# Kernel optimization log

Hardware: AMD Instinct MI355X
Metric: run time of the kernel (lower is better)

Reference implementation:

```python
import jax, jax.numpy as jnp
import numpy as np

B, N, F, H, M = 128, 512, 63, 128, 2  # batch of trees, nodes/tree (post-order), feat dim, hidden, n modules
IN = F + 1            # features + treatment scalar
GATE_IN = IN + 2 * H  # cat(input, left_hidden, right_hidden)


def _build_tree(n, seed=0):
    """Random binary tree (forest) in post-order: children indices < parent index; -1 = absent."""
    rng = np.random.default_rng(seed)
    left = -np.ones(n, np.int32)
    right = -np.ones(n, np.int32)
    roots = []
    for t in range(n):
        r = rng.random()
        if len(roots) >= 2 and r < 0.6:
            right[t] = roots.pop()
            left[t] = roots.pop()
        elif len(roots) >= 1 and r < 0.85:
            left[t] = roots.pop()
        roots.append(t)
    return jnp.asarray(left), jnp.asarray(right)


def setup_inputs() -> dict:
    key = jax.random.key(0)
    k = jax.random.split(key, 8)
    left_child, right_child = _build_tree(N, seed=0)
    scale = 0.05
    return {
        "features": jax.random.normal(k[0], (B, N, F), jnp.float32),
        "treatment_id": jax.random.uniform(k[1], (B,), jnp.float32),
        "W_gate": jax.random.normal(k[2], (M, GATE_IN, 5 * H), jnp.float32) * scale,
        "b_gate": jax.random.normal(k[3], (M, 5 * H), jnp.float32) * scale,
        "W_out": jax.random.normal(k[4], (M, H, 1), jnp.float32) * scale,
        "b_out": jax.random.normal(k[5], (M, 1), jnp.float32) * scale,
        "module_idx": jax.random.randint(k[6], (B, N), 0, M, jnp.int32),
        "left_child": left_child,
        "right_child": right_child,
    }


def reference(features, treatment_id, W_gate, b_gate, W_out, b_out,
              module_idx, left_child, right_child):
    b_, n_, f_ = features.shape
    h = W_gate.shape[-1] // 5
    batch = jnp.arange(b_)
    # input tensor = cat(features, treatment) per node  -> [B, N, F+1]
    x = jnp.concatenate(
        [features, jnp.broadcast_to(treatment_id[:, None, None], (b_, n_, 1))], axis=-1)

    def fetch(buf, idx):
        # buf: [B, N, H]; idx: scalar child index (-1 -> zeros, matching torch zero init)
        v = buf[:, jnp.maximum(idx, 0)]
        return jnp.where(idx >= 0, v, jnp.zeros_like(v))

    def step(carry, xs):
        h_buf, c_buf = carry
        x_t, mod_t, lc, rc, t = xs  # x_t [B, IN], mod_t [B], lc/rc/t scalars
        lh, lcell = fetch(h_buf, lc), fetch(c_buf, lc)
        rh, rcell = fetch(h_buf, rc), fetch(c_buf, rc)
        combined = jnp.concatenate([x_t, lh, rh], axis=-1)  # [B, GATE_IN]
        # compute gates for all modules, select per-node module (per-operator fc_gate)
        gates = (jnp.einsum('bi,mio->bmo', combined, W_gate) + b_gate)[batch, mod_t]  # [B,5H]
        i_g, fl_g, fr_g, o_g, c_hat = jnp.split(gates, 5, axis=-1)
        cell = (jax.nn.sigmoid(i_g) * jnp.tanh(c_hat)
                + jax.nn.sigmoid(fl_g) * lcell
                + jax.nn.sigmoid(fr_g) * rcell)
        hidden = jax.nn.sigmoid(o_g) * jnp.tanh(cell)
        out = (jnp.einsum('bh,mh->bm', hidden, W_out[..., 0]) + b_out[:, 0][None])[batch, mod_t]
        h_buf = jax.lax.dynamic_update_slice(h_buf, hidden[:, None, :], (0, t, 0))
        c_buf = jax.lax.dynamic_update_slice(c_buf, cell[:, None, :], (0, t, 0))
        return (h_buf, c_buf), out

    xs = (jnp.swapaxes(x, 0, 1),          # [N, B, IN]
          jnp.swapaxes(module_idx, 0, 1),  # [N, B]
          left_child, right_child, jnp.arange(n_, dtype=jnp.int32))
    init = (jnp.zeros((b_, n_, h), features.dtype), jnp.zeros((b_, n_, h), features.dtype))
    _, outs = jax.lax.scan(step, init, xs)  # outs: [N, B]
    return outs.T  # [B, N] per-node scalar outputs in post-order
```

## Files before the change

kernel.cpp:

```cpp
#include <hip/hip_runtime.h>
#include <stdint.h>

#define BB 128
#define NN 512
#define FF 63
#define HH 128
#define C5H 640
#define MM 2
#define TPB 640
#define KK4 40
#define WP_DW_PER_M (KK4 * C5H * 4)
#define WP_DWORDS (MM * WP_DW_PER_M)
#define SCAP 32
#define NLDSG 6
#define NRREG 8
#define TT 16
#define GX_OFF ((size_t)4 << 20)
#define GX_BYTES ((size_t)BB * NN * C5H * 4)

__device__ __forceinline__ uint32_t f2bf_rne(float f) {
    uint32_t u = __float_as_uint(f);
    return (u + 0x7fffu + ((u >> 16) & 1u)) >> 16;
}
__device__ __forceinline__ float sigm_f(float x) { return 1.0f / (1.0f + __expf(-x)); }
__device__ __forceinline__ float tanh_f(float x) { return 1.0f - 2.0f / (__expf(2.0f * x) + 1.0f); }

__global__ void pack_w_kernel(const float* __restrict__ Wg, uint32_t* __restrict__ Wp) {
    int i = blockIdx.x * blockDim.x + threadIdx.x;
    if (i >= WP_DWORDS) return;
    int m   = i / WP_DW_PER_M;
    int d   = i % WP_DW_PER_M;
    int p   = d & 3;
    int col = (d >> 2) % C5H;
    int kk4 = d / (C5H * 4);
    int kk  = kk4 * 4 + p;
    float w0 = Wg[((size_t)m * 320 + 2 * kk    ) * C5H + col];
    float w1 = Wg[((size_t)m * 320 + 2 * kk + 1) * C5H + col];
    Wp[i] = f2bf_rne(w0) | (f2bf_rne(w1) << 16);
}

#define DOT2(acc, w, x) asm("v_dot2_f32_bf16 %0, %1, %2, %0" : "+v"(acc) : "v"(w), "v"(x))
#define DOT4G(acc, wq, xp) do { uint4 _x = *(const uint4*)(xp); \
    DOT2(acc, (wq).x, _x.x); DOT2(acc, (wq).y, _x.y); \
    DOT2(acc, (wq).z, _x.z); DOT2(acc, (wq).w, _x.w); } while (0)

#define BAR_L()  do { asm volatile("s_waitcnt lgkmcnt(0)" ::: "memory"); \
                      __builtin_amdgcn_s_barrier(); \
                      asm volatile("" ::: "memory"); } while (0)

__device__ __forceinline__ float seg_dot(float acc, const uint4* __restrict__ w4,
                                         int g0, int ng, const uint32_t* __restrict__ cf) {
#pragma unroll 4
    for (int g = 0; g < ng; ++g) {
        uint4 w = w4[(size_t)(g0 + g) * C5H];
        uint4 x = *(const uint4*)(cf + 4 * g);
        DOT2(acc, w.x, x.x);
        DOT2(acc, w.y, x.y);
        DOT2(acc, w.z, x.z);
        DOT2(acc, w.w, x.w);
    }
    return acc;
}

__global__ __launch_bounds__(TPB, 1) void gx_kernel(
    const float* __restrict__ feat, const float* __restrict__ treat,
    const float* __restrict__ bgate, const int* __restrict__ modidx,
    const uint32_t* __restrict__ Wp, float* __restrict__ gx)
{
    __shared__ __align__(16) uint32_t comb16[TT][32];
    __shared__ int mod16[TT];
    const int tid = threadIdx.x;
    const int b   = blockIdx.x;
    const int t0  = blockIdx.y * TT;
    const float trt = treat[b];

    uint4 wx0[8], wx1[8];
    {
        const uint4* w40 = (const uint4*)Wp + tid;
        const uint4* w41 = (const uint4*)Wp + (size_t)KK4 * C5H + tid;
#pragma unroll
        for (int g = 0; g < 8; ++g) wx0[g] = w40[(size_t)g * C5H];
#pragma unroll
        for (int g = 0; g < 8; ++g) wx1[g] = w41[(size_t)g * C5H];
    }
    if (tid < TT * 32) {
        int tt = tid >> 5, l = tid & 31;
        const float* fr = feat + ((size_t)b * NN + t0 + tt) * FF;
        float a = fr[2 * l];
        float c = (l == 31) ? trt : fr[2 * l + 1];
        comb16[tt][l] = f2bf_rne(a) | (f2bf_rne(c) << 16);
    }
    if (tid < TT) mod16[tid] = modidx[b * NN + t0 + tid];
    __syncthreads();

    const float bg0 = bgate[tid], bg1 = bgate[C5H + tid];
    for (int tt = 0; tt < TT; ++tt) {
        const int m = mod16[tt];
        float acc;
        if (m == 0) {
            acc = bg0;
#pragma unroll
            for (int g = 0; g < 8; ++g) DOT4G(acc, wx0[g], &comb16[tt][4 * g]);
        } else {
            acc = bg1;
#pragma unroll
            for (int g = 0; g < 8; ++g) DOT4G(acc, wx1[g], &comb16[tt][4 * g]);
        }
        gx[((size_t)b * NN + t0 + tt) * C5H + tid] = acc;
    }
}

template<int USEGX>
__global__ __launch_bounds__(TPB, 1) void tree_lstm_kernel(
    const float* __restrict__ feat, const float* __restrict__ treat,
    const float* __restrict__ bgate, const float* __restrict__ wout,
    const float* __restrict__ bout, const int* __restrict__ modidx,
    const int* __restrict__ lchild, const int* __restrict__ rchild,
    const uint32_t* __restrict__ Wp, const float* __restrict__ gx,
    float* __restrict__ out)
{
    __shared__ __align__(16) ushort h_live[SCAP * HH];
    __shared__ float               c_live[SCAP * HH];
    __shared__ uint32_t wlds[MM][NLDSG][4][C5H];
    __shared__ float gatesf[C5H];
    __shared__ float partial[HH];
    __shared__ float wo_l[MM * HH];
    __shared__ float bo_l[MM];
    __shared__ unsigned char code_l[NN];
    __shared__ __align__(16) uint32_t comb_x[USEGX ? 4 : 32];
    __shared__ float bg_l[USEGX ? 1 : MM * C5H];

    const int tid = threadIdx.x;
    const int b   = blockIdx.x;
    const float trt = treat[b];

    for (int i = tid; i < MM * HH; i += TPB) wo_l[i] = wout[i];
    if (tid < MM) bo_l[tid] = bout[tid];
    if (!USEGX) { for (int i = tid; i < MM * C5H; i += TPB) bg_l[i] = bgate[i]; }
    for (int i = tid; i < NN; i += TPB) {
        int lc = lchild[i], rc = rchild[i];
        code_l[i] = (unsigned char)((modidx[b * NN + i] & 1) |
                                    ((lc >= 0) ? 2 : 0) | ((rc >= 0) ? 4 : 0));
    }
    for (int i = tid; i < MM * NLDSG * 4 * C5H; i += TPB) {
        int m  = i / (NLDSG * 4 * C5H);
        int r  = i % (NLDSG * 4 * C5H);
        int j  = r / (4 * C5H);
        int p  = (r / C5H) & 3;
        int c  = r % C5H;
        wlds[m][j][p][c] =
            Wp[(size_t)m * WP_DW_PER_M + (size_t)(8 + j) * 2560 + c * 4 + p];
    }

    uint4 wr0[NRREG], wr1[NRREG];
    {
        const uint4* w40 = (const uint4*)Wp + tid;
        const uint4* w41 = (const uint4*)Wp + (size_t)KK4 * C5H + tid;
#pragma unroll
        for (int j = 0; j < NRREG; ++j) wr0[j] = w40[(size_t)(24 + j) * C5H];
#pragma unroll
        for (int j = 0; j < NRREG; ++j) wr1[j] = w41[(size_t)(24 + j) * C5H];
    }

    float fx0 = 0.f, fx1 = 0.f;
    if (!USEGX && tid < 32) {
        fx0 = feat[(size_t)b * NN * FF + 2 * tid];
        if (tid < 31) fx1 = feat[(size_t)b * NN * FF + 2 * tid + 1];
    }
    const float* gxp = gx + (size_t)b * NN * C5H + tid;
    float gx_next = USEGX ? gxp[0] : 0.f;
    __syncthreads();

    int sp = 0;
    for (int t = 0; t < NN; ++t) {
        const int code = code_l[t];
        const int m = code & 1;
        const bool hasL = (code & 2) != 0, hasR = (code & 4) != 0;
        const int rh_slot = sp - 1;
        const int lh_slot = hasR ? sp - 2 : sp - 1;
        const int new_slot = hasL ? lh_slot : sp;

        if (!USEGX) {
            if (tid < 32) {
                comb_x[tid] = f2bf_rne(fx0) | (f2bf_rne((tid == 31) ? trt : fx1) << 16);
                if (t + 1 < NN) {
                    fx0 = feat[((size_t)b * NN + t + 1) * FF + 2 * tid];
                    if (tid < 31) fx1 = feat[((size_t)b * NN + t + 1) * FF + 2 * tid + 1];
                }
            }
            BAR_L();
        }

        {
            const uint4* w4 = (const uint4*)Wp + (size_t)m * (KK4 * C5H) + tid;
            float acc;
            if (USEGX) {
                acc = gx_next;
                if (t + 1 < NN) gx_next = gxp[(size_t)(t + 1) * C5H];
            } else {
                acc = bg_l[m * C5H + tid];
                acc = seg_dot(acc, w4, 0, 8, comb_x);
            }
            if (hasL) {
                const uint32_t* hl = (const uint32_t*)&h_live[lh_slot * HH];
                const uint32_t* wt = &wlds[m][0][0][0] + tid;
#pragma unroll
                for (int j = 0; j < NLDSG; ++j) {
                    uint4 w;
                    w.x = wt[(size_t)(4 * j    ) * C5H];
                    w.y = wt[(size_t)(4 * j + 1) * C5H];
                    w.z = wt[(size_t)(4 * j + 2) * C5H];
                    w.w = wt[(size_t)(4 * j + 3) * C5H];
                    DOT4G(acc, w, hl + 4 * j);
                }
                acc = seg_dot(acc, w4, 8 + NLDSG, 16 - NLDSG, hl + 4 * NLDSG);
            }
            if (hasR) {
                const uint32_t* hr = (const uint32_t*)&h_live[rh_slot * HH];
                if (m == 0) {
#pragma unroll
                    for (int j = 0; j < NRREG; ++j) DOT4G(acc, wr0[j], hr + 4 * j);
                } else {
#pragma unroll
                    for (int j = 0; j < NRREG; ++j) DOT4G(acc, wr1[j], hr + 4 * j);
                }
                acc = seg_dot(acc, w4, 24 + NRREG, 16 - NRREG, hr + 4 * NRREG);
            }
            gatesf[tid] = (tid < 4 * HH) ? sigm_f(acc) : tanh_f(acc);
        }
        BAR_L();

        if (tid < HH) {
            float s_i  = gatesf[tid];
            float s_fl = gatesf[HH + tid];
            float s_fr = gatesf[2 * HH + tid];
            float s_o  = gatesf[3 * HH + tid];
            float th   = gatesf[4 * HH + tid];
            float pcl = hasL ? c_live[lh_slot * HH + tid] : 0.0f;
            float pcr = hasR ? c_live[rh_slot * HH + tid] : 0.0f;
            float cell = s_i * th + s_fl * pcl + s_fr * pcr;
            float hid  = s_o * tanh_f(cell);
            c_live[new_slot * HH + tid] = cell;
            h_live[new_slot * HH + tid] = (ushort)f2bf_rne(hid);
            partial[tid] = hid * wo_l[m * HH + tid];
        }
        BAR_L();

        if (tid < 64) {
            float s = partial[tid] + partial[tid + 64];
#pragma unroll
            for (int off = 32; off; off >>= 1) s += __shfl_down(s, off, 64);
            if (tid == 0) out[(size_t)b * NN + t] = s + bo_l[m];
        }

        sp = hasR ? sp - 1 : (hasL ? sp : sp + 1);
    }
}

extern "C" void kernel_launch(void* const* d_in, const int* in_sizes, int n_in,
                              void* d_out, int out_size, void* d_ws, size_t ws_size,
                              hipStream_t stream) {
    const float* feat   = (const float*)d_in[0];
    const float* treat  = (const float*)d_in[1];
    const float* Wg     = (const float*)d_in[2];
    const float* bgate  = (const float*)d_in[3];
    const float* wout   = (const float*)d_in[4];
    const float* bout   = (const float*)d_in[5];
    const int*   modidx = (const int*)d_in[6];
    const int*   lchild = (const int*)d_in[7];
    const int*   rchild = (const int*)d_in[8];

    uint32_t* Wp = (uint32_t*)d_ws;
    float* gxbuf = (float*)((char*)d_ws + GX_OFF);
    float* out = (float*)d_out;
    const bool use_gx = ws_size >= GX_OFF + GX_BYTES;

    pack_w_kernel<<<(WP_DWORDS + 255) / 256, 256, 0, stream>>>(Wg, Wp);
    if (use_gx) {
        gx_kernel<<<dim3(BB, NN / TT), TPB, 0, stream>>>(feat, treat, bgate, modidx, Wp, gxbuf);
        tree_lstm_kernel<1><<<BB, TPB, 0, stream>>>(feat, treat, bgate, wout, bout,
                                                    modidx, lchild, rchild, Wp, gxbuf, out);
    } else {
        tree_lstm_kernel<0><<<BB, TPB, 0, stream>>>(feat, treat, bgate, wout, bout,
                                                    modidx, lchild, rchild, Wp, gxbuf, out);
    }
}
```

Before: 863.1 us.

## Defer output projection out of recurrent loop, store hidden to gx scratch

In the precomputed-gx path, each step now writes its hidden vector into the gx row it has already consumed, and the per-node output dot product runs in a parallel pass after the loop. This takes the reduction and its shuffle work off the serial critical path. The stack capacity shrinks from 32 to 20 slots, which frees LDS for one more weight group cached in shared memory in that path. The risk is overflowing the smaller stack if a tree needs more live nodes, and the later pass adds extra global traffic.

```diff
diff --git a/kernel.cpp b/kernel.cpp
--- a/kernel.cpp
+++ b/kernel.cpp
@@ -11,8 +11,7 @@
 #define KK4 40
 #define WP_DW_PER_M (KK4 * C5H * 4)
 #define WP_DWORDS (MM * WP_DW_PER_M)
-#define SCAP 32
-#define NLDSG 6
+#define SCAP 20
 #define NRREG 8
 #define TT 16
 #define GX_OFF ((size_t)4 << 20)
@@ -47,6 +46,9 @@
 #define BAR_L()  do { asm volatile("s_waitcnt lgkmcnt(0)" ::: "memory"); \
                       __builtin_amdgcn_s_barrier(); \
                       asm volatile("" ::: "memory"); } while (0)
+#define BAR_VL() do { asm volatile("s_waitcnt vmcnt(0) lgkmcnt(0)" ::: "memory"); \
+                      __builtin_amdgcn_s_barrier(); \
+                      asm volatile("" ::: "memory"); } while (0)
 
 __device__ __forceinline__ float seg_dot(float acc, const uint4* __restrict__ w4,
                                          int g0, int ng, const uint32_t* __restrict__ cf) {
@@ -116,19 +118,21 @@
     const float* __restrict__ bgate, const float* __restrict__ wout,
     const float* __restrict__ bout, const int* __restrict__ modidx,
     const int* __restrict__ lchild, const int* __restrict__ rchild,
-    const uint32_t* __restrict__ Wp, const float* __restrict__ gx,
+    const uint32_t* __restrict__ Wp, float* __restrict__ gx,
     float* __restrict__ out)
 {
+    constexpr int NL = USEGX ? 7 : 6;
+
     __shared__ __align__(16) ushort h_live[SCAP * HH];
     __shared__ float               c_live[SCAP * HH];
-    __shared__ uint32_t wlds[MM][NLDSG][4][C5H];
+    __shared__ uint32_t wlds[MM][NL][4][C5H];
     __shared__ float gatesf[C5H];
-    __shared__ float partial[HH];
     __shared__ float wo_l[MM * HH];
     __shared__ float bo_l[MM];
     __shared__ unsigned char code_l[NN];
     __shared__ __align__(16) uint32_t comb_x[USEGX ? 4 : 32];
     __shared__ float bg_l[USEGX ? 1 : MM * C5H];
+    __shared__ float partial[USEGX ? 1 : HH];
 
     const int tid = threadIdx.x;
     const int b   = blockIdx.x;
@@ -142,9 +146,9 @@
         code_l[i] = (unsigned char)((modidx[b * NN + i] & 1) |
                                     ((lc >= 0) ? 2 : 0) | ((rc >= 0) ? 4 : 0));
     }
-    for (int i = tid; i < MM * NLDSG * 4 * C5H; i += TPB) {
-        int m  = i / (NLDSG * 4 * C5H);
-        int r  = i % (NLDSG * 4 * C5H);
+    for (int i = tid; i < MM * NL * 4 * C5H; i += TPB) {
+        int m  = i / (NL * 4 * C5H);
+        int r  = i % (NL * 4 * C5H);
         int j  = r / (4 * C5H);
         int p  = (r / C5H) & 3;
         int c  = r % C5H;
@@ -167,7 +171,7 @@
         fx0 = feat[(size_t)b * NN * FF + 2 * tid];
         if (tid < 31) fx1 = feat[(size_t)b * NN * FF + 2 * tid + 1];
     }
-    const float* gxp = gx + (size_t)b * NN * C5H + tid;
+    float* gxp = gx + (size_t)b * NN * C5H + tid;
     float gx_next = USEGX ? gxp[0] : 0.f;
     __syncthreads();
 
@@ -205,7 +209,7 @@
                 const uint32_t* hl = (const uint32_t*)&h_live[lh_slot * HH];
                 const uint32_t* wt = &wlds[m][0][0][0] + tid;
 #pragma unroll
-                for (int j = 0; j < NLDSG; ++j) {
+                for (int j = 0; j < NL; ++j) {
                     uint4 w;
                     w.x = wt[(size_t)(4 * j    ) * C5H];
                     w.y = wt[(size_t)(4 * j + 1) * C5H];
@@ -213,7 +217,7 @@
                     w.w = wt[(size_t)(4 * j + 3) * C5H];
                     DOT4G(acc, w, hl + 4 * j);
                 }
-                acc = seg_dot(acc, w4, 8 + NLDSG, 16 - NLDSG, hl + 4 * NLDSG);
+                acc = seg_dot(acc, w4, 8 + NL, 16 - NL, hl + 4 * NL);
             }
             if (hasR) {
                 const uint32_t* hr = (const uint32_t*)&h_live[rh_slot * HH];
@@ -242,18 +246,41 @@
             float hid  = s_o * tanh_f(cell);
             c_live[new_slot * HH + tid] = cell;
             h_live[new_slot * HH + tid] = (ushort)f2bf_rne(hid);
-            partial[tid] = hid * wo_l[m * HH + tid];
+            if (USEGX) {
+                __builtin_nontemporal_store(hid, &gxp[(size_t)t * C5H]);
+            } else {
+                partial[tid] = hid * wo_l[m * HH + tid];
+            }
         }
         BAR_L();
 
-        if (tid < 64) {
-            float s = partial[tid] + partial[tid + 64];
+        if (!USEGX) {
+            if (tid < 64) {
+                float s = partial[tid] + partial[tid + 64];
+#pragma unroll
+                for (int off = 32; off; off >>= 1) s += __shfl_down(s, off, 64);
+                if (tid == 0) out[(size_t)b * NN + t] = s + bo_l[m];
+            }
+        }
+
+        sp = hasR ? sp - 1 : (hasL ? sp : sp + 1);
+    }
+
+    if (USEGX) {
+        BAR_VL();
+        const int wave = tid >> 6, lane = tid & 63;
+        const float* gxh = gx + (size_t)b * NN * C5H;
+        for (int t = wave; t < NN; t += TPB / 64) {
+            const int m = code_l[t] & 1;
+            float h0 = __builtin_nontemporal_load(&gxh[(size_t)t * C5H + lane]);
+            float h1 = __builtin_nontemporal_load(&gxh[(size_t)t * C5H + 64 + lane]);
+            float p0 = __fmul_rn(h0, wo_l[m * HH + lane]);
+            float p1 = __fmul_rn(h1, wo_l[m * HH + 64 + lane]);
+            float s  = __fadd_rn(p0, p1);
 #pragma unroll
             for (int off = 32; off; off >>= 1) s += __shfl_down(s, off, 64);
-            if (tid == 0) out[(size_t)b * NN + t] = s + bo_l[m];
-        }
-
-        sp = hasR ? sp - 1 : (hasL ? sp : sp + 1);
+            if (lane == 0) out[(size_t)b * NN + t] = s + bo_l[m];
+        }
     }
 }
 
```

After: 845.4 us. 2.1% less time.
